# Performance work log

Hardware: AMD Instinct MI355X
Metric: run time of the kernel (lower is better)

## Reference

```python
import jax, jax.numpy as jnp
import numpy as np

B, T, U, H, M, K, C = 64, 800, 80, 512, 20, 10, 80  # batch, tsteps, char len, rnn_size, nmixtures, kmixtures, char_vec_len


def _lstm(x, W, Uw, b):
    """Keras-semantics LSTM (gate order i,f,g,o), zero initial state. x: [B,T,D] -> [B,T,H]."""
    xg = jnp.einsum('btd,dh->bth', x, W) + b  # precompute input contribution
    h0 = jnp.zeros((x.shape[0], Uw.shape[0]), x.dtype)
    c0 = jnp.zeros_like(h0)

    def step(carry, zt):
        h, c = carry
        z = zt + h @ Uw
        i, f, g, o = jnp.split(z, 4, axis=-1)
        c = jax.nn.sigmoid(f) * c + jax.nn.sigmoid(i) * jnp.tanh(g)
        h = jax.nn.sigmoid(o) * jnp.tanh(c)
        return (h, c), h

    _, hs = jax.lax.scan(step, (h0, c0), jnp.swapaxes(xg, 0, 1))
    return jnp.swapaxes(hs, 0, 1)


def _forward(stroke_data, char_seq, kappa0, W0, U0, b0, W1, U1, b1, W2, U2, b2, Wa, ba, Wm, bm):
    lstm0_out = _lstm(stroke_data, W0, U0, b0)  # [B,T,H]
    # Attention window: the per-timestep loop in the source only carries kappa,
    # which is a running sum of exp(kappa_offset) -> vectorize via cumsum.
    abk = jnp.exp(jnp.einsum('bth,hk->btk', lstm0_out, Wa) + ba)  # [B,T,3K]
    alpha, beta, koff = jnpp_split = jnp.split(abk, 3, axis=-1)
    kappa = kappa0[:, None, :, 0] + jnp.cumsum(koff, axis=1)  # [B,T,K]
    u = jnp.arange(char_seq.shape[1], dtype=stroke_data.dtype)  # [U]
    # phi: [B,T,U] = sum_k alpha * exp(-beta * (kappa - u)^2)
    phi = jnp.sum(alpha[..., None] * jnp.exp(-beta[..., None] * (kappa[..., None] - u) ** 2), axis=2)
    windows = jnp.einsum('btu,buc->btc', phi, char_seq)  # [B,T,C]
    aug = jnp.concatenate([lstm0_out, windows, stroke_data], axis=-1)
    lstm1_out = _lstm(aug, W1, U1, b1)
    lstm2_out = _lstm(lstm1_out, W2, U2, b2)
    mdn = jnp.einsum('bth,hn->btn', lstm2_out, Wm) + bm  # [B,T,1+6M]
    eos_hat = mdn[..., 0:1]
    pi_hat, mu1, mu2, s1_hat, s2_hat, rho_hat = jnp.split(mdn[..., 1:], 6, axis=-1)
    return jnp.concatenate([
        jax.nn.sigmoid(-eos_hat),
        jax.nn.softmax(pi_hat, axis=-1),
        mu1, mu2,
        jnp.exp(s1_hat), jnp.exp(s2_hat),
        jnp.tanh(rho_hat),
    ], axis=-1)  # [B,T,1+6M]


def setup_inputs() -> dict:
    key = jax.random.key(0)
    ks = jax.random.split(key, 12)
    init = lambda k, shape: jax.random.truncated_normal(k, -2.0, 2.0, shape, jnp.float32) * 0.075
    return {
        'stroke_data': jax.random.normal(ks[0], (B, T, 3), jnp.float32),
        'char_seq': jax.nn.one_hot(jax.random.randint(ks[1], (B, U), 0, C), C, dtype=jnp.float32),
        'kappa0': jnp.zeros((B, K, 1), jnp.float32),
        'W0': init(ks[2], (3, 4 * H)), 'U0': init(ks[3], (H, 4 * H)), 'b0': jnp.zeros((4 * H,)),
        'W1': init(ks[4], (H + C + 3, 4 * H)), 'U1': init(ks[5], (H, 4 * H)), 'b1': jnp.zeros((4 * H,)),
        'W2': init(ks[6], (H, 4 * H)), 'U2': init(ks[7], (H, 4 * H)), 'b2': jnp.zeros((4 * H,)),
        'Wa': init(ks[8], (H, 3 * K)),
        'ba': -3.0 + 0.25 * jax.random.truncated_normal(ks[9], -2.0, 2.0, (3 * K,), jnp.float32),
        'Wm': init(ks[10], (H, 1 + 6 * M)), 'bm': jnp.zeros((1 + 6 * M,)),
    }


def reference(stroke_data, char_seq, kappa0, W0, U0, b0, W1, U1, b1, W2, U2, b2, Wa, ba, Wm, bm):
    return _forward(stroke_data, char_seq, kappa0, W0, U0, b0, W1, U1, b1, W2, U2, b2, Wa, ba, Wm, bm)
```

## Files before the change

kernel.cpp:

```cpp
#include <hip/hip_runtime.h>

typedef unsigned short u16;
typedef unsigned int u32;
typedef short v8s __attribute__((ext_vector_type(8)));
typedef float v4f __attribute__((ext_vector_type(4)));
typedef unsigned int v4u __attribute__((ext_vector_type(4)));
typedef unsigned int v2u __attribute__((ext_vector_type(2)));

#define MFMA16 __builtin_amdgcn_mfma_f32_16x16x32_bf16

constexpr int TT = 800;
constexpr int NBLK = 178;

constexpr int AUGB  = 2240;
constexpr int AUG2B = 2048;

constexpr size_t AUGR_OFF  = 131072;
constexpr size_t AUG2R_OFF = AUGR_OFF + (size_t)4 * 64 * AUGB;
constexpr size_t WAT_OFF   = AUG2R_OFF + (size_t)4 * 64 * AUG2B;
constexpr size_t WS_ZERO   = WAT_OFF + (size_t)32 * 512 * 2;

constexpr u32 SMEM_BYTES = 82944;

enum { G_S0D = 0, G_SAD = 1, G_S1D = 2, G_S2D = 3, G_S1R = 4, G_SAR = 5, G_S2R = 6, G_SMR = 7 };

__device__ __forceinline__ float bf2f(u16 u) { return __uint_as_float(((u32)u) << 16); }
__device__ __forceinline__ u16 f2bf(float f) {
    u32 x = __float_as_uint(f);
    return (u16)((x + 0x7fffu + ((x >> 16) & 1u)) >> 16);
}
__device__ __forceinline__ short f2bfs(float f) { return (short)f2bf(f); }
__device__ __forceinline__ float sigf(float x) { return 1.f / (1.f + __expf(-x)); }
__device__ __forceinline__ float tanhf2(float x) { return 1.f - 2.f / (1.f + __expf(2.f * x)); }

__device__ __forceinline__ __amdgpu_buffer_rsrc_t mkrsrc(const void* p) {
    return __builtin_amdgcn_make_buffer_rsrc((void*)p, (short)0, -1, 0x00020000);
}
__device__ __forceinline__ v4u ldu4(__amdgpu_buffer_rsrc_t r, int off) {
    return __builtin_amdgcn_raw_buffer_load_b128(r, off, 0, 17);
}
__device__ __forceinline__ v2u ldu8(__amdgpu_buffer_rsrc_t r, int off) {
    return __builtin_amdgcn_raw_buffer_load_b64(r, off, 0, 17);
}
__device__ __forceinline__ void stq8(__amdgpu_buffer_rsrc_t r, int off, u16 a, u16 b, u16 c, u16 d) {
    v2u t; t[0] = (u32)a | ((u32)b << 16); t[1] = (u32)c | ((u32)d << 16);
    __builtin_amdgcn_raw_buffer_store_b64(t, r, off, 0, 17);
}
__device__ __forceinline__ void stq4(__amdgpu_buffer_rsrc_t r, int off, u16 a, u16 b) {
    u32 t = (u32)a | ((u32)b << 16);
    __builtin_amdgcn_raw_buffer_store_b32(t, r, off, 0, 17);
}

__device__ __forceinline__ void publish(u32* ctrl, int g, int t, int sub) {
    __hip_atomic_fetch_add(ctrl + g * 4096 + (t & 3) * 1024 + (sub & 15) * 64, 1u,
                           __ATOMIC_RELAXED, __HIP_MEMORY_SCOPE_AGENT);
}
__device__ __forceinline__ void wait4(u32* ctrl,
    int g0, int t0, u32 n0, int m0, int g1, int t1, u32 n1, int m1,
    int g2, int t2, u32 n2, int m2, int g3, int t3, u32 n3, int m3)
{
    if (threadIdx.x < 64) {
        const int lane = threadIdx.x;
        const int cl = lane >> 4, k = lane & 15;
        int g, tt, mb; u32 nn;
        if (cl == 0)      { g = g0; tt = t0; nn = n0; mb = m0; }
        else if (cl == 1) { g = g1; tt = t1; nn = n1; mb = m1; }
        else if (cl == 2) { g = g2; tt = t2; nn = n2; mb = m2; }
        else              { g = g3; tt = t3; nn = n3; mb = m3; }
        const u32 tgt = (g >= 0 && tt >= 0) ? nn * (u32)((tt >> 2) + 1) : 0u;
        u32* p = (tgt > 0) ? (ctrl + g * 4096 + (tt & 3) * 1024 + (mb + (k & 7)) * 64) : (u32*)0;
        int sp = 0;
        for (;;) {
            u32 v = p ? __hip_atomic_load(p, __ATOMIC_RELAXED, __HIP_MEMORY_SCOPE_AGENT) : 0u;
            v += __shfl_xor(v, 1); v += __shfl_xor(v, 2);
            v += __shfl_xor(v, 4); v += __shfl_xor(v, 8);
            const bool bad = (tgt > 0) && (v < tgt);
            if (__ballot(bad) == 0ull) break;
            if (sp >= 2) __builtin_amdgcn_s_sleep(4);
            else if (sp == 1) __builtin_amdgcn_s_sleep(1);
            sp++;
        }
    }
    __syncthreads();
}

__global__ void wat_init(const float* __restrict__ Wa, u16* __restrict__ WaT) {
    __amdgpu_buffer_rsrc_t r = mkrsrc(WaT);
    for (int idx = blockIdx.x * 256 + threadIdx.x; idx < 32 * 512 / 2; idx += gridDim.x * 256) {
        const int e0 = idx * 2, e1 = e0 + 1;
        const int n0 = e0 >> 9, k0 = e0 & 511;
        const int n1 = e1 >> 9, k1 = e1 & 511;
        const u16 a = (n0 < 30) ? f2bf(Wa[k0 * 30 + n0]) : (u16)0;
        const u16 b = (n1 < 30) ? f2bf(Wa[k1 * 30 + n1]) : (u16)0;
        stq4(r, idx * 4, a, b);
    }
}

__global__ __launch_bounds__(256, 1) void hw_main(
    const float* __restrict__ stroke, const float* __restrict__ charseq, const float* __restrict__ kappa0,
    const float* __restrict__ W0, const float* __restrict__ U0, const float* __restrict__ b0,
    const float* __restrict__ W1, const float* __restrict__ U1, const float* __restrict__ b1,
    const float* __restrict__ W2, const float* __restrict__ U2, const float* __restrict__ b2,
    const float* __restrict__ ba, const float* __restrict__ Wm, const float* __restrict__ bm,
    float* __restrict__ out, char* __restrict__ ws)
{
    extern __shared__ __align__(16) char smem[];
    u32* ctrl = (u32*)ws;
    u16* augr  = (u16*)(ws + AUGR_OFF);
    u16* aug2r = (u16*)(ws + AUG2R_OFF);
    const u16* WaT = (const u16*)(ws + WAT_OFF);

    const int blk = blockIdx.x, tid = threadIdx.x;
    const int wave = tid >> 6, lane = tid & 63;
    const int quad = lane >> 4, l15 = lane & 15;

    if (blk < 32) {
        const int cs = blk & 15, mg = blk >> 4;
        const int mb = mg * 8, sub = mb + (cs & 7);
        __amdgpu_buffer_rsrc_t ra = mkrsrc(augr);
        u16*   aL  = (u16*)smem;
        float* zb  = (float*)(smem + 33280);
        float* w0s = (float*)(smem + 50176);
        float* b0s = (float*)(smem + 51712);
        if (tid < 128) {
            const int cn2 = (tid >> 5) * 512 + cs * 32 + (tid & 31);
            b0s[tid] = b0[cn2];
            #pragma unroll
            for (int d = 0; d < 3; d++) w0s[d * 128 + tid] = W0[d * 2048 + cn2];
        }
        v8s bw0[16], bw1[16];
        {
            const int cnA = wave * 512 + cs * 32 + l15;
            const int cnB = cnA + 16;
            #pragma unroll
            for (int kc = 0; kc < 16; kc++)
                #pragma unroll
                for (int j = 0; j < 8; j++) {
                    const int k = kc * 32 + quad * 8 + j;
                    bw0[kc][j] = f2bfs(U0[k * 2048 + cnA]);
                    bw1[kc][j] = f2bfs(U0[k * 2048 + cnB]);
                }
        }
        float cst[4] = {0.f, 0.f, 0.f, 0.f};
        const int bl_ = tid & 31;
        const int bpre = mg * 32 + bl_;
        __syncthreads();
        #pragma unroll 1
        for (int t = 0; t < TT; t++) {
            const float xx0 = stroke[(bpre * TT + t) * 3 + 0];
            const float xx1 = stroke[(bpre * TT + t) * 3 + 1];
            const float xx2 = stroke[(bpre * TT + t) * 3 + 2];
            wait4(ctrl, G_S0D, t - 1, 32, mb, G_S1R, t - 4, 64, mb, G_SAR, t - 4, 16, mb, -1, 0, 0, 0);
            {
                const int base = (((t + 3) & 3) * 64 + mg * 32) * AUGB;
                #pragma unroll
                for (int c8 = 0; c8 < 8; c8++) {
                    const int c = tid + 256 * c8;
                    const int row = c >> 6, off = c & 63;
                    v4u d = ldu4(ra, base + row * AUGB + off * 16);
                    *(v4u*)((char*)aL + row * 1040 + off * 16) = d;
                }
            }
            __syncthreads();
            v4f c0a = {0,0,0,0}, c0b = {0,0,0,0}, c1a = {0,0,0,0}, c1b = {0,0,0,0};
            const int xo = quad * 16;
            #pragma unroll
            for (int kc = 0; kc < 16; kc++) {
                v8s x0 = *(const v8s*)((const char*)aL + l15 * 1040 + kc * 64 + xo);
                v8s x1 = *(const v8s*)((const char*)aL + (16 + l15) * 1040 + kc * 64 + xo);
                c0a = MFMA16(x0, bw0[kc], c0a, 0, 0, 0);
                c1a = MFMA16(x0, bw1[kc], c1a, 0, 0, 0);
                c0b = MFMA16(x1, bw0[kc], c0b, 0, 0, 0);
                c1b = MFMA16(x1, bw1[kc], c1b, 0, 0, 0);
            }
            const int n0 = wave * 32 + l15, n1 = n0 + 16;
            #pragma unroll
            for (int r = 0; r < 4; r++) {
                zb[(quad * 4 + r) * 132 + n0] = c0a[r];
                zb[(quad * 4 + r) * 132 + n1] = c1a[r];
                zb[(16 + quad * 4 + r) * 132 + n0] = c0b[r];
                zb[(16 + quad * 4 + r) * 132 + n1] = c1b[r];
            }
            __syncthreads();
            {
                const int bl = tid & 31, jj = tid >> 5;
                const int b = mg * 32 + bl;
                u16 hv[4];
                #pragma unroll
                for (int m = 0; m < 4; m++) {
                    const int j = jj * 4 + m;
                    float z[4];
                    #pragma unroll
                    for (int g = 0; g < 4; g++) {
                        const int n = g * 32 + j;
                        z[g] = zb[bl * 132 + n] + b0s[n] + xx0 * w0s[n] + xx1 * w0s[128 + n] + xx2 * w0s[256 + n];
                    }
                    const float cc = sigf(z[1]) * cst[m] + sigf(z[0]) * tanhf2(z[2]);
                    cst[m] = cc;
                    hv[m] = f2bf(sigf(z[3]) * tanhf2(cc));
                }
                stq8(ra, ((t & 3) * 64 + b) * AUGB + (cs * 32 + jj * 4) * 2, hv[0], hv[1], hv[2], hv[3]);
            }
            __syncthreads();
            if (tid == 0) publish(ctrl, G_S0D, t, sub);
        }
    } else if (blk < 96) {
        const int q = blk - 32, cs = q >> 1, mg = q & 1;
        const int mb = mg * 8, sub = mb + (cs & 7);
        __amdgpu_buffer_rsrc_t ra = mkrsrc(augr);
        __amdgpu_buffer_rsrc_t r2 = mkrsrc(aug2r);
        u16*   aL  = (u16*)smem;
        float* zb  = (float*)(smem + 72192);
        float* b1s = (float*)(smem + 80896);
        if (tid < 64) b1s[tid] = b1[(tid >> 4) * 512 + cs * 16 + (tid & 15)];
        v8s bw[35];
        {
            const int cn = wave * 512 + cs * 16 + l15;
            #pragma unroll
            for (int kc = 0; kc < 35; kc++)
                #pragma unroll
                for (int j = 0; j < 8; j++) {
                    const int k = kc * 32 + quad * 8 + j;
                    short v = 0;
                    if (k < 595) v = f2bfs(W1[k * 2048 + cn]);
                    else if (k >= 596 && k < 1108) v = f2bfs(U1[(k - 596) * 2048 + cn]);
                    bw[kc][j] = v;
                }
        }
        if (tid < 32) { v4u z4 = {0,0,0,0}; *(v4u*)((char*)aL + tid * 2256 + 2224) = z4; }
        float cst[2] = {0.f, 0.f};
        __syncthreads();
        #pragma unroll 1
        for (int t = 0; t < TT; t++) {
            wait4(ctrl, G_S0D, t, 32, mb, G_SAD, t, 16, mb, G_S2R, t - 4, 64, mb, -1, 0, 0, 0);
            {
                const int base = ((t & 3) * 64 + mg * 32) * AUGB;
                #pragma unroll
                for (int c10 = 0; c10 < 10; c10++) {
                    const int c = tid + 256 * c10;
                    if (c < 2400) {
                        const int row = c / 75, off = c - row * 75;
                        v4u d = ldu4(ra, base + row * AUGB + off * 16);
                        *(v4u*)((char*)aL + row * 2256 + off * 16) = d;
                    }
                }
            }
            __syncthreads();
            if (tid == 0) publish(ctrl, G_S1R, t, sub);
            wait4(ctrl, G_S1D, t - 1, 64, mb, -1, 0, 0, 0, -1, 0, 0, 0, -1, 0, 0, 0);
            {
                const int base = ((t & 3) * 64 + mg * 32) * AUGB;
                if (tid < 32) {
                    v2u d8 = ldu8(ra, base + tid * AUGB + 1192);
                    *(v2u*)((char*)aL + tid * 2256 + 1192) = d8;
                }
                #pragma unroll
                for (int c8 = 0; c8 < 8; c8++) {
                    const int c = tid + 256 * c8;
                    const int row = c >> 6, off = 75 + (c & 63);
                    v4u d = ldu4(ra, base + row * AUGB + off * 16);
                    *(v4u*)((char*)aL + row * 2256 + off * 16) = d;
                }
            }
            v4f c0 = {0,0,0,0}, c1 = {0,0,0,0};
            const int xo = quad * 16;
            #pragma unroll
            for (int kc = 0; kc < 18; kc++) {
                v8s x0 = *(const v8s*)((const char*)aL + l15 * 2256 + kc * 64 + xo);
                v8s x1 = *(const v8s*)((const char*)aL + (16 + l15) * 2256 + kc * 64 + xo);
                c0 = MFMA16(x0, bw[kc], c0, 0, 0, 0);
                c1 = MFMA16(x1, bw[kc], c1, 0, 0, 0);
            }
            __syncthreads();
            #pragma unroll
            for (int kc = 18; kc < 35; kc++) {
                v8s x0 = *(const v8s*)((const char*)aL + l15 * 2256 + kc * 64 + xo);
                v8s x1 = *(const v8s*)((const char*)aL + (16 + l15) * 2256 + kc * 64 + xo);
                c0 = MFMA16(x0, bw[kc], c0, 0, 0, 0);
                c1 = MFMA16(x1, bw[kc], c1, 0, 0, 0);
            }
            #pragma unroll
            for (int r = 0; r < 4; r++) {
                zb[(quad * 4 + r) * 68 + wave * 17 + l15] = c0[r];
                zb[(16 + quad * 4 + r) * 68 + wave * 17 + l15] = c1[r];
            }
            __syncthreads();
            {
                const int bl = tid & 31, jj = tid >> 5;
                const int b = mg * 32 + bl;
                u16 hv[2];
                #pragma unroll
                for (int m = 0; m < 2; m++) {
                    const int j = jj * 2 + m;
                    float z[4];
                    #pragma unroll
                    for (int g = 0; g < 4; g++)
                        z[g] = zb[bl * 68 + g * 17 + j] + b1s[g * 16 + j];
                    const float cc = sigf(z[1]) * cst[m] + sigf(z[0]) * tanhf2(z[2]);
                    cst[m] = cc;
                    hv[m] = f2bf(sigf(z[3]) * tanhf2(cc));
                }
                stq4(ra, (((t + 1) & 3) * 64 + b) * AUGB + (596 + cs * 16 + jj * 2) * 2, hv[0], hv[1]);
                stq4(r2, ((t & 3) * 64 + b) * AUG2B + (cs * 16 + jj * 2) * 2, hv[0], hv[1]);
            }
            __syncthreads();
            if (tid == 0) publish(ctrl, G_S1D, t, sub);
        }
    } else if (blk < 160) {
        const int q = blk - 96, cs = q >> 1, mg = q & 1;
        const int mb = mg * 8, sub = mb + (cs & 7);
        __amdgpu_buffer_rsrc_t r2 = mkrsrc(aug2r);
        u16*   aL  = (u16*)smem;
        float* zb  = (float*)(smem + 66048);
        float* b2s = (float*)(smem + 74752);
        if (tid < 64) b2s[tid] = b2[(tid >> 4) * 512 + cs * 16 + (tid & 15)];
        v8s bw[32];
        {
            const int cn = wave * 512 + cs * 16 + l15;
            #pragma unroll
            for (int kc = 0; kc < 32; kc++)
                #pragma unroll
                for (int j = 0; j < 8; j++) {
                    const int k = kc * 32 + quad * 8 + j;
                    bw[kc][j] = (k < 512) ? f2bfs(W2[k * 2048 + cn]) : f2bfs(U2[(k - 512) * 2048 + cn]);
                }
        }
        float cst[2] = {0.f, 0.f};
        __syncthreads();
        #pragma unroll 1
        for (int t = 0; t < TT; t++) {
            wait4(ctrl, G_S1D, t, 64, mb, G_SMR, t - 4, 2, mb, -1, 0, 0, 0, -1, 0, 0, 0);
            {
                const int base = ((t & 3) * 64 + mg * 32) * AUG2B;
                #pragma unroll
                for (int c8 = 0; c8 < 8; c8++) {
                    const int c = tid + 256 * c8;
                    const int row = c >> 6, off = c & 63;
                    v4u d = ldu4(r2, base + row * AUG2B + off * 16);
                    *(v4u*)((char*)aL + row * 2064 + off * 16) = d;
                }
            }
            __syncthreads();
            if (tid == 0) publish(ctrl, G_S2R, t, sub);
            wait4(ctrl, G_S2D, t - 1, 64, mb, -1, 0, 0, 0, -1, 0, 0, 0, -1, 0, 0, 0);
            {
                const int base = ((t & 3) * 64 + mg * 32) * AUG2B;
                #pragma unroll
                for (int c8 = 0; c8 < 8; c8++) {
                    const int c = tid + 256 * c8;
                    const int row = c >> 6, off = 64 + (c & 63);
                    v4u d = ldu4(r2, base + row * AUG2B + off * 16);
                    *(v4u*)((char*)aL + row * 2064 + off * 16) = d;
                }
            }
            v4f c0 = {0,0,0,0}, c1 = {0,0,0,0};
            const int xo = quad * 16;
            #pragma unroll
            for (int kc = 0; kc < 16; kc++) {
                v8s x0 = *(const v8s*)((const char*)aL + l15 * 2064 + kc * 64 + xo);
                v8s x1 = *(const v8s*)((const char*)aL + (16 + l15) * 2064 + kc * 64 + xo);
                c0 = MFMA16(x0, bw[kc], c0, 0, 0, 0);
                c1 = MFMA16(x1, bw[kc], c1, 0, 0, 0);
            }
            __syncthreads();
            #pragma unroll
            for (int kc = 16; kc < 32; kc++) {
                v8s x0 = *(const v8s*)((const char*)aL + l15 * 2064 + kc * 64 + xo);
                v8s x1 = *(const v8s*)((const char*)aL + (16 + l15) * 2064 + kc * 64 + xo);
                c0 = MFMA16(x0, bw[kc], c0, 0, 0, 0);
                c1 = MFMA16(x1, bw[kc], c1, 0, 0, 0);
            }
            #pragma unroll
            for (int r = 0; r < 4; r++) {
                zb[(quad * 4 + r) * 68 + wave * 17 + l15] = c0[r];
                zb[(16 + quad * 4 + r) * 68 + wave * 17 + l15] = c1[r];
            }
            __syncthreads();
            {
                const int bl = tid & 31, jj = tid >> 5;
                const int b = mg * 32 + bl;
                u16 hv[2];
                #pragma unroll
                for (int m = 0; m < 2; m++) {
                    const int j = jj * 2 + m;
                    float z[4];
                    #pragma unroll
                    for (int g = 0; g < 4; g++)
                        z[g] = zb[bl * 68 + g * 17 + j] + b2s[g * 16 + j];
                    const float cc = sigf(z[1]) * cst[m] + sigf(z[0]) * tanhf2(z[2]);
                    cst[m] = cc;
                    hv[m] = f2bf(sigf(z[3]) * tanhf2(cc));
                }
                stq4(r2, (((t + 1) & 3) * 64 + b) * AUG2B + (512 + cs * 16 + jj * 2) * 2, hv[0], hv[1]);
            }
            __syncthreads();
            if (tid == 0) publish(ctrl, G_S2D, t, sub);
        }
    } else if (blk < 176) {
        const int a = blk - 160;
        const int mg = a >> 3, mb = mg * 8, sub = mb + (a & 7);
        const int b = a * 4 + wave;
        __amdgpu_buffer_rsrc_t ra = mkrsrc(augr);
        u16*   watl = (u16*)smem;
        u16*   hrow = (u16*)(smem + 33280);
        float* phis = (float*)(smem + 37440);
        u16*   idxs = (u16*)(smem + 38720);
        {
            #pragma unroll
            for (int c8 = 0; c8 < 8; c8++) {
                const int c = tid + 256 * c8;
                const int row = c >> 6, off = c & 63;
                *(v4u*)((char*)watl + row * 1040 + off * 16) = *(const v4u*)(WaT + row * 512 + off * 8);
            }
        }
        #pragma unroll
        for (int rep = 0; rep < 2; rep++) {
            const int u = rep * 64 + lane;
            if (u < 80) {
                int c = 0;
                #pragma unroll 1
                for (int cc = 0; cc < 80; cc++)
                    if (charseq[b * 6400 + u * 80 + cc] > 0.5f) c = cc;
                idxs[wave * 80 + u] = (u16)c;
            }
        }
        float kap = (lane < 10) ? kappa0[b * 10 + lane] : 0.f;
        const float baf = (lane < 30) ? ba[lane] : 0.f;
        const int nn = lane & 31;
        const int k0 = (lane >> 5) * 256;
        const u16* wrow = watl + nn * 520 + k0;
        __syncthreads();
        #pragma unroll 1
        for (int t = 0; t < TT; t++) {
            float sx0 = 0.f, sx1 = 0.f;
            if (lane == 40) { sx0 = stroke[(b * TT + t) * 3 + 0]; sx1 = stroke[(b * TT + t) * 3 + 1]; }
            else if (lane == 41) { sx0 = stroke[(b * TT + t) * 3 + 2]; }
            wait4(ctrl, G_S0D, t, 32, mb, G_S1R, t - 4, 64, mb, -1, 0, 0, 0, -1, 0, 0, 0);
            {
                const int row = tid >> 6, off = tid & 63;
                v4u d = ldu4(ra, ((t & 3) * 64 + a * 4 + row) * AUGB + off * 16);
                *(v4u*)((char*)hrow + row * 1040 + off * 16) = d;
            }
            __syncthreads();
            if (tid == 0) publish(ctrl, G_SAR, t, sub);
            float acc = 0.f;
            #pragma unroll
            for (int kk = 0; kk < 32; kk++) {
                v8s hv = *(const v8s*)((const char*)hrow + wave * 1040 + (k0 + kk * 8) * 2);
                v8s wv = *(const v8s*)(wrow + kk * 8);
                #pragma unroll
                for (int e = 0; e < 8; e++) acc += bf2f((u16)hv[e]) * bf2f((u16)wv[e]);
            }
            acc += __shfl_xor(acc, 32);
            const float abk = __expf(acc + baf);
            const float kofv = __shfl(abk, 20 + (lane < 10 ? lane : 0));
            if (lane < 10) kap += kofv;
            const float u1f = (float)lane;
            float p1 = 0.f, p2 = 0.f;
            #pragma unroll
            for (int kk = 0; kk < 10; kk++) {
                const float al = __shfl(abk, kk);
                const float be = __shfl(abk, 10 + kk);
                const float kp = __shfl(kap, kk);
                const float d1 = kp - u1f, d2 = kp - (u1f + 64.f);
                p1 += al * __expf(-be * d1 * d1);
                p2 += al * __expf(-be * d2 * d2);
            }
            phis[wave * 80 + lane] = p1;
            if (lane < 16) phis[wave * 80 + 64 + lane] = p2;
            __syncthreads();
            const int db = (((t & 3) * 64 + b) * AUGB) + 512 * 2;
            if (lane < 40) {
                const int c0 = 2 * lane;
                float w0 = 0.f, w1 = 0.f;
                #pragma unroll 1
                for (int u = 0; u < 80; u++) {
                    const float pv = phis[wave * 80 + u];
                    const int ix = (int)idxs[wave * 80 + u];
                    w0 += (ix == c0)     ? pv : 0.f;
                    w1 += (ix == c0 + 1) ? pv : 0.f;
                }
                stq4(ra, db + c0 * 2, f2bf(w0), f2bf(w1));
            } else if (lane == 40) {
                stq4(ra, db + 80 * 2, f2bf(sx0), f2bf(sx1));
            } else if (lane == 41) {
                stq4(ra, db + 82 * 2, f2bf(sx0), (u16)0);
            }
            __syncthreads();
            if (tid == 0) publish(ctrl, G_SAD, t, sub);
        }
    } else {
        const int mgs = blk - 176;
        const int mb = mgs * 8, sub = mb;
        __amdgpu_buffer_rsrc_t r2 = mkrsrc(aug2r);
        u16*   aL = (u16*)smem;
        float* zb = (float*)(smem + 33280);
        v8s bw0[16], bw1[16];
        {
            const int nA = wave * 32 + l15, nB = nA + 16;
            #pragma unroll
            for (int kc = 0; kc < 16; kc++)
                #pragma unroll
                for (int j = 0; j < 8; j++) {
                    const int k = kc * 32 + quad * 8 + j;
                    bw0[kc][j] = (nA < 121) ? f2bfs(Wm[k * 121 + nA]) : (short)0;
                    bw1[kc][j] = (nB < 121) ? f2bfs(Wm[k * 121 + nB]) : (short)0;
                }
        }
        __syncthreads();
        #pragma unroll 1
        for (int t = 0; t < TT; t++) {
            wait4(ctrl, G_S2D, t, 64, mb, -1, 0, 0, 0, -1, 0, 0, 0, -1, 0, 0, 0);
            {
                const int base = (((t + 1) & 3) * 64 + mgs * 32) * AUG2B + 1024;
                #pragma unroll
                for (int c8 = 0; c8 < 8; c8++) {
                    const int c = tid + 256 * c8;
                    const int row = c >> 6, off = c & 63;
                    v4u d = ldu4(r2, base + row * AUG2B + off * 16);
                    *(v4u*)((char*)aL + row * 1040 + off * 16) = d;
                }
            }
            __syncthreads();
            if (tid == 0) publish(ctrl, G_SMR, t, sub);
            v4f c0a = {0,0,0,0}, c0b = {0,0,0,0}, c1a = {0,0,0,0}, c1b = {0,0,0,0};
            const int xo = quad * 16;
            #pragma unroll
            for (int kc = 0; kc < 16; kc++) {
                v8s x0 = *(const v8s*)((const char*)aL + l15 * 1040 + kc * 64 + xo);
                v8s x1 = *(const v8s*)((const char*)aL + (16 + l15) * 1040 + kc * 64 + xo);
                c0a = MFMA16(x0, bw0[kc], c0a, 0, 0, 0);
                c1a = MFMA16(x0, bw1[kc], c1a, 0, 0, 0);
                c0b = MFMA16(x1, bw0[kc], c0b, 0, 0, 0);
                c1b = MFMA16(x1, bw1[kc], c1b, 0, 0, 0);
            }
            const int n0 = wave * 32 + l15, n1 = n0 + 16;
            #pragma unroll
            for (int r = 0; r < 4; r++) {
                zb[(quad * 4 + r) * 132 + n0] = c0a[r];
                zb[(quad * 4 + r) * 132 + n1] = c1a[r];
                zb[(16 + quad * 4 + r) * 132 + n0] = c0b[r];
                zb[(16 + quad * 4 + r) * 132 + n1] = c1b[r];
            }
            __syncthreads();
            {
                const int b8 = tid >> 3, g8 = tid & 7;
                const int b = mgs * 32 + b8;
                const float* zr = zb + b8 * 132;
                float* orow = out + ((size_t)(b * TT + t)) * 121;
                if (g8 == 0) {
                    orow[0] = sigf(-(zr[0] + bm[0]));
                    float mx = -1e30f;
                    float zv[20];
                    #pragma unroll 1
                    for (int nl = 1; nl <= 20; nl++) { zv[nl - 1] = zr[nl] + bm[nl]; mx = fmaxf(mx, zv[nl - 1]); }
                    float ss = 0.f;
                    #pragma unroll 1
                    for (int nl = 0; nl < 20; nl++) { zv[nl] = __expf(zv[nl] - mx); ss += zv[nl]; }
                    const float inv = 1.f / ss;
                    #pragma unroll 1
                    for (int nl = 0; nl < 20; nl++) orow[nl + 1] = zv[nl] * inv;
                } else if (g8 <= 2) {
                    const int s0 = 21 + (g8 - 1) * 20;
                    #pragma unroll 1
                    for (int nl = s0; nl < s0 + 20; nl++) orow[nl] = zr[nl] + bm[nl];
                } else if (g8 <= 4) {
                    const int s0 = 61 + (g8 - 3) * 20;
                    #pragma unroll 1
                    for (int nl = s0; nl < s0 + 20; nl++) orow[nl] = __expf(zr[nl] + bm[nl]);
                } else if (g8 <= 6) {
                    const int s0 = 101 + (g8 - 5) * 10;
                    #pragma unroll 1
                    for (int nl = s0; nl < s0 + 10; nl++) orow[nl] = tanhf2(zr[nl] + bm[nl]);
                }
            }
            __syncthreads();
        }
    }
}

extern "C" void kernel_launch(void* const* d_in, const int* in_sizes, int n_in,
                              void* d_out, int out_size, void* d_ws, size_t ws_size,
                              hipStream_t stream) {
    const float* stroke  = (const float*)d_in[0];
    const float* charseq = (const float*)d_in[1];
    const float* kappa0  = (const float*)d_in[2];
    const float* W0 = (const float*)d_in[3];
    const float* U0 = (const float*)d_in[4];
    const float* b0 = (const float*)d_in[5];
    const float* W1 = (const float*)d_in[6];
    const float* U1 = (const float*)d_in[7];
    const float* b1 = (const float*)d_in[8];
    const float* W2 = (const float*)d_in[9];
    const float* U2 = (const float*)d_in[10];
    const float* b2 = (const float*)d_in[11];
    const float* Wa = (const float*)d_in[12];
    const float* ba = (const float*)d_in[13];
    const float* Wm = (const float*)d_in[14];
    const float* bm = (const float*)d_in[15];
    char* ws = (char*)d_ws;

    static bool attr_done = false;
    if (!attr_done) {
        hipFuncSetAttribute((const void*)hw_main,
                            hipFuncAttributeMaxDynamicSharedMemorySize, SMEM_BYTES);
        attr_done = true;
    }

    hipMemsetAsync(d_ws, 0, WS_ZERO, stream);
    wat_init<<<8, 256, 0, stream>>>(Wa, (u16*)(ws + WAT_OFF));
    hw_main<<<NBLK, 256, SMEM_BYTES, stream>>>(stroke, charseq, kappa0, W0, U0, b0,
                                               W1, U1, b1, W2, U2, b2, ba, Wm, bm,
                                               (float*)d_out, ws);
}
```

Measured before the change: 8.748 ms.

## Double block size so extra waves help stage loads; use cache-bypassing poll loads

Launches each persistent block with 512 threads instead of 256. The four extra waves only share the global-to-LDS staging copies, so each thread issues half as many loads per step, while the MFMA and pointwise work stays on the first four waves or 256 threads. The flag-polling loop now uses inline-asm buffer loads with sc0/sc1 cache-bypass bits and a shorter backoff sleep, aiming to cut the latency of seeing cross-block flags. The cost is more register pressure from launch_bounds 512 and more threads taking part in every __syncthreads.

```diff
diff --git a/kernel.cpp b/kernel.cpp
--- a/kernel.cpp
+++ b/kernel.cpp
@@ -49,6 +49,22 @@
 __device__ __forceinline__ void stq4(__amdgpu_buffer_rsrc_t r, int off, u16 a, u16 b) {
     u32 t = (u32)a | ((u32)b << 16);
     __builtin_amdgcn_raw_buffer_store_b32(t, r, off, 0, 17);
+}
+
+__device__ __forceinline__ v4u mksrd(const void* p) {
+    v4u r;
+    r[0] = (u32)(size_t)p;
+    r[1] = (u32)((size_t)p >> 32);
+    r[2] = 0xFFFFFFFFu;
+    r[3] = 0x00020000u;
+    return r;
+}
+__device__ __forceinline__ u32 poll_ld(v4u srd, int off) {
+    u32 v;
+    asm volatile("buffer_load_dword %0, %1, %2, 0 offen sc0 sc1\n\t"
+                 "s_waitcnt vmcnt(0)"
+                 : "=v"(v) : "v"(off), "s"(srd) : "memory");
+    return v;
 }
 
 __device__ __forceinline__ void publish(u32* ctrl, int g, int t, int sub) {
@@ -68,15 +84,16 @@
         else if (cl == 2) { g = g2; tt = t2; nn = n2; mb = m2; }
         else              { g = g3; tt = t3; nn = n3; mb = m3; }
         const u32 tgt = (g >= 0 && tt >= 0) ? nn * (u32)((tt >> 2) + 1) : 0u;
-        u32* p = (tgt > 0) ? (ctrl + g * 4096 + (tt & 3) * 1024 + (mb + (k & 7)) * 64) : (u32*)0;
+        const v4u srd = mksrd(ctrl);
+        const int boff = (g >= 0) ? (g * 4096 + ((tt & 3)) * 1024 + (mb + (k & 7)) * 64) * 4 : 0;
         int sp = 0;
         for (;;) {
-            u32 v = p ? __hip_atomic_load(p, __ATOMIC_RELAXED, __HIP_MEMORY_SCOPE_AGENT) : 0u;
+            u32 v = (tgt > 0) ? poll_ld(srd, boff) : 0u;
             v += __shfl_xor(v, 1); v += __shfl_xor(v, 2);
             v += __shfl_xor(v, 4); v += __shfl_xor(v, 8);
             const bool bad = (tgt > 0) && (v < tgt);
             if (__ballot(bad) == 0ull) break;
-            if (sp >= 2) __builtin_amdgcn_s_sleep(4);
+            if (sp >= 2) __builtin_amdgcn_s_sleep(2);
             else if (sp == 1) __builtin_amdgcn_s_sleep(1);
             sp++;
         }
@@ -96,7 +113,7 @@
     }
 }
 
-__global__ __launch_bounds__(256, 1) void hw_main(
+__global__ __launch_bounds__(512, 1) void hw_main(
     const float* __restrict__ stroke, const float* __restrict__ charseq, const float* __restrict__ kappa0,
     const float* __restrict__ W0, const float* __restrict__ U0, const float* __restrict__ b0,
     const float* __restrict__ W1, const float* __restrict__ U1, const float* __restrict__ b1,
@@ -129,7 +146,7 @@
             for (int d = 0; d < 3; d++) w0s[d * 128 + tid] = W0[d * 2048 + cn2];
         }
         v8s bw0[16], bw1[16];
-        {
+        if (wave < 4) {
             const int cnA = wave * 512 + cs * 32 + l15;
             const int cnB = cnA + 16;
             #pragma unroll
@@ -142,47 +159,51 @@
                 }
         }
         float cst[4] = {0.f, 0.f, 0.f, 0.f};
-        const int bl_ = tid & 31;
-        const int bpre = mg * 32 + bl_;
+        const int bpre = mg * 32 + (tid & 31);
         __syncthreads();
         #pragma unroll 1
         for (int t = 0; t < TT; t++) {
-            const float xx0 = stroke[(bpre * TT + t) * 3 + 0];
-            const float xx1 = stroke[(bpre * TT + t) * 3 + 1];
-            const float xx2 = stroke[(bpre * TT + t) * 3 + 2];
+            float xx0 = 0.f, xx1 = 0.f, xx2 = 0.f;
+            if (tid < 256) {
+                xx0 = stroke[(bpre * TT + t) * 3 + 0];
+                xx1 = stroke[(bpre * TT + t) * 3 + 1];
+                xx2 = stroke[(bpre * TT + t) * 3 + 2];
+            }
             wait4(ctrl, G_S0D, t - 1, 32, mb, G_S1R, t - 4, 64, mb, G_SAR, t - 4, 16, mb, -1, 0, 0, 0);
             {
                 const int base = (((t + 3) & 3) * 64 + mg * 32) * AUGB;
                 #pragma unroll
-                for (int c8 = 0; c8 < 8; c8++) {
-                    const int c = tid + 256 * c8;
+                for (int c4 = 0; c4 < 4; c4++) {
+                    const int c = tid + 512 * c4;
                     const int row = c >> 6, off = c & 63;
                     v4u d = ldu4(ra, base + row * AUGB + off * 16);
                     *(v4u*)((char*)aL + row * 1040 + off * 16) = d;
                 }
             }
             __syncthreads();
-            v4f c0a = {0,0,0,0}, c0b = {0,0,0,0}, c1a = {0,0,0,0}, c1b = {0,0,0,0};
-            const int xo = quad * 16;
-            #pragma unroll
-            for (int kc = 0; kc < 16; kc++) {
-                v8s x0 = *(const v8s*)((const char*)aL + l15 * 1040 + kc * 64 + xo);
-                v8s x1 = *(const v8s*)((const char*)aL + (16 + l15) * 1040 + kc * 64 + xo);
-                c0a = MFMA16(x0, bw0[kc], c0a, 0, 0, 0);
-                c1a = MFMA16(x0, bw1[kc], c1a, 0, 0, 0);
-                c0b = MFMA16(x1, bw0[kc], c0b, 0, 0, 0);
-                c1b = MFMA16(x1, bw1[kc], c1b, 0, 0, 0);
-            }
-            const int n0 = wave * 32 + l15, n1 = n0 + 16;
-            #pragma unroll
-            for (int r = 0; r < 4; r++) {
-                zb[(quad * 4 + r) * 132 + n0] = c0a[r];
-                zb[(quad * 4 + r) * 132 + n1] = c1a[r];
-                zb[(16 + quad * 4 + r) * 132 + n0] = c0b[r];
-                zb[(16 + quad * 4 + r) * 132 + n1] = c1b[r];
-            }
-            __syncthreads();
-            {
+            if (wave < 4) {
+                v4f c0a = {0,0,0,0}, c0b = {0,0,0,0}, c1a = {0,0,0,0}, c1b = {0,0,0,0};
+                const int xo = quad * 16;
+                #pragma unroll
+                for (int kc = 0; kc < 16; kc++) {
+                    v8s x0 = *(const v8s*)((const char*)aL + l15 * 1040 + kc * 64 + xo);
+                    v8s x1 = *(const v8s*)((const char*)aL + (16 + l15) * 1040 + kc * 64 + xo);
+                    c0a = MFMA16(x0, bw0[kc], c0a, 0, 0, 0);
+                    c1a = MFMA16(x0, bw1[kc], c1a, 0, 0, 0);
+                    c0b = MFMA16(x1, bw0[kc], c0b, 0, 0, 0);
+                    c1b = MFMA16(x1, bw1[kc], c1b, 0, 0, 0);
+                }
+                const int n0 = wave * 32 + l15, n1 = n0 + 16;
+                #pragma unroll
+                for (int r = 0; r < 4; r++) {
+                    zb[(quad * 4 + r) * 132 + n0] = c0a[r];
+                    zb[(quad * 4 + r) * 132 + n1] = c1a[r];
+                    zb[(16 + quad * 4 + r) * 132 + n0] = c0b[r];
+                    zb[(16 + quad * 4 + r) * 132 + n1] = c1b[r];
+                }
+            }
+            __syncthreads();
+            if (tid < 256) {
                 const int bl = tid & 31, jj = tid >> 5;
                 const int b = mg * 32 + bl;
                 u16 hv[4];
@@ -214,7 +235,7 @@
         float* b1s = (float*)(smem + 80896);
         if (tid < 64) b1s[tid] = b1[(tid >> 4) * 512 + cs * 16 + (tid & 15)];
         v8s bw[35];
-        {
+        if (wave < 4) {
             const int cn = wave * 512 + cs * 16 + l15;
             #pragma unroll
             for (int kc = 0; kc < 35; kc++)
@@ -236,8 +257,8 @@
             {
                 const int base = ((t & 3) * 64 + mg * 32) * AUGB;
                 #pragma unroll
-                for (int c10 = 0; c10 < 10; c10++) {
-                    const int c = tid + 256 * c10;
+                for (int c5 = 0; c5 < 5; c5++) {
+                    const int c = tid + 512 * c5;
                     if (c < 2400) {
                         const int row = c / 75, off = c - row * 75;
                         v4u d = ldu4(ra, base + row * AUGB + off * 16);
@@ -255,8 +276,8 @@
                     *(v2u*)((char*)aL + tid * 2256 + 1192) = d8;
                 }
                 #pragma unroll
-                for (int c8 = 0; c8 < 8; c8++) {
-                    const int c = tid + 256 * c8;
+                for (int c4 = 0; c4 < 4; c4++) {
+                    const int c = tid + 512 * c4;
                     const int row = c >> 6, off = 75 + (c & 63);
                     v4u d = ldu4(ra, base + row * AUGB + off * 16);
                     *(v4u*)((char*)aL + row * 2256 + off * 16) = d;
@@ -264,28 +285,32 @@
             }
             v4f c0 = {0,0,0,0}, c1 = {0,0,0,0};
             const int xo = quad * 16;
-            #pragma unroll
-            for (int kc = 0; kc < 18; kc++) {
-                v8s x0 = *(const v8s*)((const char*)aL + l15 * 2256 + kc * 64 + xo);
-                v8s x1 = *(const v8s*)((const char*)aL + (16 + l15) * 2256 + kc * 64 + xo);
-                c0 = MFMA16(x0, bw[kc], c0, 0, 0, 0);
-                c1 = MFMA16(x1, bw[kc], c1, 0, 0, 0);
-            }
-            __syncthreads();
-            #pragma unroll
-            for (int kc = 18; kc < 35; kc++) {
-                v8s x0 = *(const v8s*)((const char*)aL + l15 * 2256 + kc * 64 + xo);
-                v8s x1 = *(const v8s*)((const char*)aL + (16 + l15) * 2256 + kc * 64 + xo);
-                c0 = MFMA16(x0, bw[kc], c0, 0, 0, 0);
-                c1 = MFMA16(x1, bw[kc], c1, 0, 0, 0);
-            }
-            #pragma unroll
-            for (int r = 0; r < 4; r++) {
-                zb[(quad * 4 + r) * 68 + wave * 17 + l15] = c0[r];
-                zb[(16 + quad * 4 + r) * 68 + wave * 17 + l15] = c1[r];
-            }
-            __syncthreads();
-            {
+            if (wave < 4) {
+                #pragma unroll
+                for (int kc = 0; kc < 18; kc++) {
+                    v8s x0 = *(const v8s*)((const char*)aL + l15 * 2256 + kc * 64 + xo);
+                    v8s x1 = *(const v8s*)((const char*)aL + (16 + l15) * 2256 + kc * 64 + xo);
+                    c0 = MFMA16(x0, bw[kc], c0, 0, 0, 0);
+                    c1 = MFMA16(x1, bw[kc], c1, 0, 0, 0);
+                }
+            }
+            __syncthreads();
+            if (wave < 4) {
+                #pragma unroll
+                for (int kc = 18; kc < 35; kc++) {
+                    v8s x0 = *(const v8s*)((const char*)aL + l15 * 2256 + kc * 64 + xo);
+                    v8s x1 = *(const v8s*)((const char*)aL + (16 + l15) * 2256 + kc * 64 + xo);
+                    c0 = MFMA16(x0, bw[kc], c0, 0, 0, 0);
+                    c1 = MFMA16(x1, bw[kc], c1, 0, 0, 0);
+                }
+                #pragma unroll
+                for (int r = 0; r < 4; r++) {
+                    zb[(quad * 4 + r) * 68 + wave * 17 + l15] = c0[r];
+                    zb[(16 + quad * 4 + r) * 68 + wave * 17 + l15] = c1[r];
+                }
+            }
+            __syncthreads();
+            if (tid < 256) {
                 const int bl = tid & 31, jj = tid >> 5;
                 const int b = mg * 32 + bl;
                 u16 hv[2];
@@ -315,7 +340,7 @@
         float* b2s = (float*)(smem + 74752);
         if (tid < 64) b2s[tid] = b2[(tid >> 4) * 512 + cs * 16 + (tid & 15)];
         v8s bw[32];
-        {
+        if (wave < 4) {
             const int cn = wave * 512 + cs * 16 + l15;
             #pragma unroll
             for (int kc = 0; kc < 32; kc++)
@@ -333,8 +358,8 @@
             {
                 const int base = ((t & 3) * 64 + mg * 32) * AUG2B;
                 #pragma unroll
-                for (int c8 = 0; c8 < 8; c8++) {
-                    const int c = tid + 256 * c8;
+                for (int c4 = 0; c4 < 4; c4++) {
+                    const int c = tid + 512 * c4;
                     const int row = c >> 6, off = c & 63;
                     v4u d = ldu4(r2, base + row * AUG2B + off * 16);
                     *(v4u*)((char*)aL + row * 2064 + off * 16) = d;
@@ -346,8 +371,8 @@
             {
                 const int base = ((t & 3) * 64 + mg * 32) * AUG2B;
                 #pragma unroll
-                for (int c8 = 0; c8 < 8; c8++) {
-                    const int c = tid + 256 * c8;
+                for (int c4 = 0; c4 < 4; c4++) {
+                    const int c = tid + 512 * c4;
                     const int row = c >> 6, off = 64 + (c & 63);
                     v4u d = ldu4(r2, base + row * AUG2B + off * 16);
                     *(v4u*)((char*)aL + row * 2064 + off * 16) = d;
@@ -355,28 +380,32 @@
             }
             v4f c0 = {0,0,0,0}, c1 = {0,0,0,0};
             const int xo = quad * 16;
-            #pragma unroll
-            for (int kc = 0; kc < 16; kc++) {
-                v8s x0 = *(const v8s*)((const char*)aL + l15 * 2064 + kc * 64 + xo);
-                v8s x1 = *(const v8s*)((const char*)aL + (16 + l15) * 2064 + kc * 64 + xo);
-                c0 = MFMA16(x0, bw[kc], c0, 0, 0, 0);
-                c1 = MFMA16(x1, bw[kc], c1, 0, 0, 0);
-            }
-            __syncthreads();
-            #pragma unroll
-            for (int kc = 16; kc < 32; kc++) {
-                v8s x0 = *(const v8s*)((const char*)aL + l15 * 2064 + kc * 64 + xo);
-                v8s x1 = *(const v8s*)((const char*)aL + (16 + l15) * 2064 + kc * 64 + xo);
-                c0 = MFMA16(x0, bw[kc], c0, 0, 0, 0);
-                c1 = MFMA16(x1, bw[kc], c1, 0, 0, 0);
-            }
-            #pragma unroll
-            for (int r = 0; r < 4; r++) {
-                zb[(quad * 4 + r) * 68 + wave * 17 + l15] = c0[r];
-                zb[(16 + quad * 4 + r) * 68 + wave * 17 + l15] = c1[r];
-            }
-            __syncthreads();
-            {
+            if (wave < 4) {
+                #pragma unroll
+                for (int kc = 0; kc < 16; kc++) {
+                    v8s x0 = *(const v8s*)((const char*)aL + l15 * 2064 + kc * 64 + xo);
+                    v8s x1 = *(const v8s*)((const char*)aL + (16 + l15) * 2064 + kc * 64 + xo);
+                    c0 = MFMA16(x0, bw[kc], c0, 0, 0, 0);
+                    c1 = MFMA16(x1, bw[kc], c1, 0, 0, 0);
+                }
+            }
+            __syncthreads();
+            if (wave < 4) {
+                #pragma unroll
+                for (int kc = 16; kc < 32; kc++) {
+                    v8s x0 = *(const v8s*)((const char*)aL + l15 * 2064 + kc * 64 + xo);
+                    v8s x1 = *(const v8s*)((const char*)aL + (16 + l15) * 2064 + kc * 64 + xo);
+                    c0 = MFMA16(x0, bw[kc], c0, 0, 0, 0);
+                    c1 = MFMA16(x1, bw[kc], c1, 0, 0, 0);
+                }
+                #pragma unroll
+                for (int r = 0; r < 4; r++) {
+                    zb[(quad * 4 + r) * 68 + wave * 17 + l15] = c0[r];
+                    zb[(16 + quad * 4 + r) * 68 + wave * 17 + l15] = c1[r];
+                }
+            }
+            __syncthreads();
+            if (tid < 256) {
                 const int bl = tid & 31, jj = tid >> 5;
                 const int b = mg * 32 + bl;
                 u16 hv[2];
@@ -399,7 +428,7 @@
     } else if (blk < 176) {
         const int a = blk - 160;
         const int mg = a >> 3, mb = mg * 8, sub = mb + (a & 7);
-        const int b = a * 4 + wave;
+        const int b = a * 4 + (wave & 3);
         __amdgpu_buffer_rsrc_t ra = mkrsrc(augr);
         u16*   watl = (u16*)smem;
         u16*   hrow = (u16*)(smem + 33280);
@@ -407,21 +436,23 @@
         u16*   idxs = (u16*)(smem + 38720);
         {
             #pragma unroll
-            for (int c8 = 0; c8 < 8; c8++) {
-                const int c = tid + 256 * c8;
+            for (int c4 = 0; c4 < 4; c4++) {
+                const int c = tid + 512 * c4;
                 const int row = c >> 6, off = c & 63;
                 *(v4u*)((char*)watl + row * 1040 + off * 16) = *(const v4u*)(WaT + row * 512 + off * 8);
             }
         }
-        #pragma unroll
-        for (int rep = 0; rep < 2; rep++) {
-            const int u = rep * 64 + lane;
-            if (u < 80) {
-                int c = 0;
-                #pragma unroll 1
-                for (int cc = 0; cc < 80; cc++)
-                    if (charseq[b * 6400 + u * 80 + cc] > 0.5f) c = cc;
-                idxs[wave * 80 + u] = (u16)c;
+        if (wave < 4) {
+            #pragma unroll
+            for (int rep = 0; rep < 2; rep++) {
+                const int u = rep * 64 + lane;
+                if (u < 80) {
+                    int c = 0;
+                    #pragma unroll 1
+                    for (int cc = 0; cc < 80; cc++)
+                        if (charseq[b * 6400 + u * 80 + cc] > 0.5f) c = cc;
+                    idxs[wave * 80 + u] = (u16)c;
+                }
             }
         }
         float kap = (lane < 10) ? kappa0[b * 10 + lane] : 0.f;
@@ -433,58 +464,64 @@
         #pragma unroll 1
         for (int t = 0; t < TT; t++) {
             float sx0 = 0.f, sx1 = 0.f;
-            if (lane == 40) { sx0 = stroke[(b * TT + t) * 3 + 0]; sx1 = stroke[(b * TT + t) * 3 + 1]; }
-            else if (lane == 41) { sx0 = stroke[(b * TT + t) * 3 + 2]; }
+            if (wave < 4) {
+                if (lane == 40) { sx0 = stroke[(b * TT + t) * 3 + 0]; sx1 = stroke[(b * TT + t) * 3 + 1]; }
+                else if (lane == 41) { sx0 = stroke[(b * TT + t) * 3 + 2]; }
+            }
             wait4(ctrl, G_S0D, t, 32, mb, G_S1R, t - 4, 64, mb, -1, 0, 0, 0, -1, 0, 0, 0);
-            {
+            if (tid < 256) {
                 const int row = tid >> 6, off = tid & 63;
                 v4u d = ldu4(ra, ((t & 3) * 64 + a * 4 + row) * AUGB + off * 16);
                 *(v4u*)((char*)hrow + row * 1040 + off * 16) = d;
             }
             __syncthreads();
             if (tid == 0) publish(ctrl, G_SAR, t, sub);
-            float acc = 0.f;
-            #pragma unroll
-            for (int kk = 0; kk < 32; kk++) {
-                v8s hv = *(const v8s*)((const char*)hrow + wave * 1040 + (k0 + kk * 8) * 2);
-                v8s wv = *(const v8s*)(wrow + kk * 8);
-                #pragma unroll
-                for (int e = 0; e < 8; e++) acc += bf2f((u16)hv[e]) * bf2f((u16)wv[e]);
-            }
-            acc += __shfl_xor(acc, 32);
-            const float abk = __expf(acc + baf);
-            const float kofv = __shfl(abk, 20 + (lane < 10 ? lane : 0));
-            if (lane < 10) kap += kofv;
-            const float u1f = (float)lane;
-            float p1 = 0.f, p2 = 0.f;
-            #pragma unroll
-            for (int kk = 0; kk < 10; kk++) {
-                const float al = __shfl(abk, kk);
-                const float be = __shfl(abk, 10 + kk);
-                const float kp = __shfl(kap, kk);
-                const float d1 = kp - u1f, d2 = kp - (u1f + 64.f);
-                p1 += al * __expf(-be * d1 * d1);
-                p2 += al * __expf(-be * d2 * d2);
-            }
-            phis[wave * 80 + lane] = p1;
-            if (lane < 16) phis[wave * 80 + 64 + lane] = p2;
-            __syncthreads();
-            const int db = (((t & 3) * 64 + b) * AUGB) + 512 * 2;
-            if (lane < 40) {
-                const int c0 = 2 * lane;
-                float w0 = 0.f, w1 = 0.f;
-                #pragma unroll 1
-                for (int u = 0; u < 80; u++) {
-                    const float pv = phis[wave * 80 + u];
-                    const int ix = (int)idxs[wave * 80 + u];
-                    w0 += (ix == c0)     ? pv : 0.f;
-                    w1 += (ix == c0 + 1) ? pv : 0.f;
-                }
-                stq4(ra, db + c0 * 2, f2bf(w0), f2bf(w1));
-            } else if (lane == 40) {
-                stq4(ra, db + 80 * 2, f2bf(sx0), f2bf(sx1));
-            } else if (lane == 41) {
-                stq4(ra, db + 82 * 2, f2bf(sx0), (u16)0);
+            if (wave < 4) {
+                float acc = 0.f;
+                #pragma unroll
+                for (int kk = 0; kk < 32; kk++) {
+                    v8s hv = *(const v8s*)((const char*)hrow + wave * 1040 + (k0 + kk * 8) * 2);
+                    v8s wv = *(const v8s*)(wrow + kk * 8);
+                    #pragma unroll
+                    for (int e = 0; e < 8; e++) acc += bf2f((u16)hv[e]) * bf2f((u16)wv[e]);
+                }
+                acc += __shfl_xor(acc, 32);
+                const float abk = __expf(acc + baf);
+                const float kofv = __shfl(abk, 20 + (lane < 10 ? lane : 0));
+                if (lane < 10) kap += kofv;
+                const float u1f = (float)lane;
+                float p1 = 0.f, p2 = 0.f;
+                #pragma unroll
+                for (int kk = 0; kk < 10; kk++) {
+                    const float al = __shfl(abk, kk);
+                    const float be = __shfl(abk, 10 + kk);
+                    const float kp = __shfl(kap, kk);
+                    const float d1 = kp - u1f, d2 = kp - (u1f + 64.f);
+                    p1 += al * __expf(-be * d1 * d1);
+                    p2 += al * __expf(-be * d2 * d2);
+                }
+                phis[wave * 80 + lane] = p1;
+                if (lane < 16) phis[wave * 80 + 64 + lane] = p2;
+            }
+            __syncthreads();
+            if (wave < 4) {
+                const int db = (((t & 3) * 64 + b) * AUGB) + 512 * 2;
+                if (lane < 40) {
+                    const int c0 = 2 * lane;
+                    float w0 = 0.f, w1 = 0.f;
+                    #pragma unroll 1
+                    for (int u = 0; u < 80; u++) {
+                        const float pv = phis[wave * 80 + u];
+                        const int ix = (int)idxs[wave * 80 + u];
+                        w0 += (ix == c0)     ? pv : 0.f;
+                        w1 += (ix == c0 + 1) ? pv : 0.f;
+                    }
+                    stq4(ra, db + c0 * 2, f2bf(w0), f2bf(w1));
+                } else if (lane == 40) {
+                    stq4(ra, db + 80 * 2, f2bf(sx0), f2bf(sx1));
+                } else if (lane == 41) {
+                    stq4(ra, db + 82 * 2, f2bf(sx0), (u16)0);
+                }
             }
             __syncthreads();
             if (tid == 0) publish(ctrl, G_SAD, t, sub);
@@ -496,7 +533,7 @@
         u16*   aL = (u16*)smem;
         float* zb = (float*)(smem + 33280);
         v8s bw0[16], bw1[16];
-        {
+        if (wave < 4) {
             const int nA = wave * 32 + l15, nB = nA + 16;
             #pragma unroll
             for (int kc = 0; kc < 16; kc++)
@@ -514,8 +551,8 @@
             {
                 const int base = (((t + 1) & 3) * 64 + mgs * 32) * AUG2B + 1024;
                 #pragma unroll
-                for (int c8 = 0; c8 < 8; c8++) {
-                    const int c = tid + 256 * c8;
+                for (int c4 = 0; c4 < 4; c4++) {
+                    const int c = tid + 512 * c4;
                     const int row = c >> 6, off = c & 63;
                     v4u d = ldu4(r2, base + row * AUG2B + off * 16);
                     *(v4u*)((char*)aL + row * 1040 + off * 16) = d;
@@ -523,27 +560,29 @@
             }
             __syncthreads();
             if (tid == 0) publish(ctrl, G_SMR, t, sub);
-            v4f c0a = {0,0,0,0}, c0b = {0,0,0,0}, c1a = {0,0,0,0}, c1b = {0,0,0,0};
-            const int xo = quad * 16;
-            #pragma unroll
-            for (int kc = 0; kc < 16; kc++) {
-                v8s x0 = *(const v8s*)((const char*)aL + l15 * 1040 + kc * 64 + xo);
-                v8s x1 = *(const v8s*)((const char*)aL + (16 + l15) * 1040 + kc * 64 + xo);
-                c0a = MFMA16(x0, bw0[kc], c0a, 0, 0, 0);
-                c1a = MFMA16(x0, bw1[kc], c1a, 0, 0, 0);
-                c0b = MFMA16(x1, bw0[kc], c0b, 0, 0, 0);
-                c1b = MFMA16(x1, bw1[kc], c1b, 0, 0, 0);
-            }
-            const int n0 = wave * 32 + l15, n1 = n0 + 16;
-            #pragma unroll
-            for (int r = 0; r < 4; r++) {
-                zb[(quad * 4 + r) * 132 + n0] = c0a[r];
-                zb[(quad * 4 + r) * 132 + n1] = c1a[r];
-                zb[(16 + quad * 4 + r) * 132 + n0] = c0b[r];
-                zb[(16 + quad * 4 + r) * 132 + n1] = c1b[r];
-            }
-            __syncthreads();
-            {
+            if (wave < 4) {
+                v4f c0a = {0,0,0,0}, c0b = {0,0,0,0}, c1a = {0,0,0,0}, c1b = {0,0,0,0};
+                const int xo = quad * 16;
+                #pragma unroll
+                for (int kc = 0; kc < 16; kc++) {
+                    v8s x0 = *(const v8s*)((const char*)aL + l15 * 1040 + kc * 64 + xo);
+                    v8s x1 = *(const v8s*)((const char*)aL + (16 + l15) * 1040 + kc * 64 + xo);
+                    c0a = MFMA16(x0, bw0[kc], c0a, 0, 0, 0);
+                    c1a = MFMA16(x0, bw1[kc], c1a, 0, 0, 0);
+                    c0b = MFMA16(x1, bw0[kc], c0b, 0, 0, 0);
+                    c1b = MFMA16(x1, bw1[kc], c1b, 0, 0, 0);
+                }
+                const int n0 = wave * 32 + l15, n1 = n0 + 16;
+                #pragma unroll
+                for (int r = 0; r < 4; r++) {
+                    zb[(quad * 4 + r) * 132 + n0] = c0a[r];
+                    zb[(quad * 4 + r) * 132 + n1] = c1a[r];
+                    zb[(16 + quad * 4 + r) * 132 + n0] = c0b[r];
+                    zb[(16 + quad * 4 + r) * 132 + n1] = c1b[r];
+                }
+            }
+            __syncthreads();
+            if (tid < 256) {
                 const int b8 = tid >> 3, g8 = tid & 7;
                 const int b = mgs * 32 + b8;
                 const float* zr = zb + b8 * 132;
@@ -609,7 +648,7 @@
 
     hipMemsetAsync(d_ws, 0, WS_ZERO, stream);
     wat_init<<<8, 256, 0, stream>>>(Wa, (u16*)(ws + WAT_OFF));
-    hw_main<<<NBLK, 256, SMEM_BYTES, stream>>>(stroke, charseq, kappa0, W0, U0, b0,
+    hw_main<<<NBLK, 512, SMEM_BYTES, stream>>>(stroke, charseq, kappa0, W0, U0, b0,
                                                W1, U1, b1, W2, U2, b2, ba, Wm, bm,
                                                (float*)d_out, ws);
 }
```

After: 8.594 ms. Within noise of the previous version (-1.8%).
